# Performance work log

Hardware: AMD Instinct MI355X
Metric: run time of the kernel (lower is better)

The kernel has to match this reference:

```python
import jax, jax.numpy as jnp
import numpy as np

BATCH, SEQ, H_IN, N_STATE, H_OUT = 16, 4096, 128, 256, 128
RMIN, RMAX, MAX_PHASE = 0.9, 1.0, 6.283


def setup_inputs() -> dict:
    key = jax.random.key(0)
    ks = jax.random.split(key, 9)
    u = jax.random.normal(ks[0], (BATCH, SEQ, H_IN), jnp.float32)
    # LRU exponential parameterization init (matches torch __init__)
    u1 = jax.random.uniform(ks[1], (N_STATE,), jnp.float32)
    u2 = jax.random.uniform(ks[2], (N_STATE,), jnp.float32)
    nu_log = jnp.log(-0.5 * jnp.log(u1 * (RMAX + RMIN) * (RMAX - RMIN) + RMIN ** 2))
    theta_log = jnp.log(MAX_PHASE * u2)
    lam_abs = jnp.exp(-jnp.exp(nu_log))
    gamma_log = jnp.log(jnp.sqrt(1.0 - lam_abs ** 2))
    s2in = np.sqrt(2.0 * H_IN).astype(np.float32)
    B_re = jax.random.normal(ks[3], (N_STATE, H_IN), jnp.float32) / s2in
    B_im = jax.random.normal(ks[4], (N_STATE, H_IN), jnp.float32) / s2in
    sst = np.sqrt(float(N_STATE)).astype(np.float32)
    C_re = jax.random.normal(ks[5], (H_OUT, N_STATE), jnp.float32) / sst
    C_im = jax.random.normal(ks[6], (H_OUT, N_STATE), jnp.float32) / sst
    D = jax.random.normal(ks[7], (H_OUT, H_IN), jnp.float32) / np.sqrt(float(H_IN)).astype(np.float32)
    return dict(u=u, nu_log=nu_log, theta_log=theta_log, gamma_log=gamma_log,
                B_re=B_re, B_im=B_im, C_re=C_re, C_im=C_im, D=D)


def _combine(a, b):
    # complex affine composition: (l, x) o (l', x') -> (l*l', l'*x + x')
    l1r, l1i, x1r, x1i = a
    l2r, l2i, x2r, x2i = b
    lr = l1r * l2r - l1i * l2i
    li = l1r * l2i + l1i * l2r
    xr = l2r * x1r - l2i * x1i + x2r
    xi = l2r * x1i + l2i * x1r + x2i
    return (lr, li, xr, xi)


def reference(u, nu_log, theta_log, gamma_log, B_re, B_im, C_re, C_im, D):
    lam_mod = jnp.exp(-jnp.exp(nu_log))          # |lambda|, [N]
    th = jnp.exp(theta_log)
    lam_re = lam_mod * jnp.cos(th)
    lam_im = lam_mod * jnp.sin(th)
    gammas = jnp.exp(gamma_log)                  # [N]
    # input projection Bu_t = gamma * (B @ u_t), complex -> real/imag parts
    Bu_re = jnp.einsum('blh,nh->bln', u, B_re) * gammas  # [B,L,N]
    Bu_im = jnp.einsum('blh,nh->bln', u, B_im) * gammas
    Bsz, L, N = Bu_re.shape
    lr = jnp.broadcast_to(lam_re, (Bsz, L, N))
    li = jnp.broadcast_to(lam_im, (Bsz, L, N))
    # parallel scan of x_t = lambda * x_{t-1} + Bu_t, x0 = 0
    _, _, xr, xi = jax.lax.associative_scan(_combine, (lr, li, Bu_re, Bu_im), axis=1)
    zero = jnp.zeros((Bsz, 1, N), u.dtype)
    pre_re = jnp.concatenate([zero, xr[:, :-1]], axis=1)  # states[:, :-1]
    pre_im = jnp.concatenate([zero, xi[:, :-1]], axis=1)
    # y_t = Re(C x_{t-1}) + D u_t
    y = (jnp.einsum('bln,on->blo', pre_re, C_re)
         - jnp.einsum('bln,on->blo', pre_im, C_im)
         + jnp.einsum('blh,oh->blo', u, D))
    return y
```

## Files before the change

### kernel.cpp

```cpp
#include <hip/hip_runtime.h>
#include <math.h>

#define BATCH 16
#define SEQ   4096
#define HIN   128
#define NST   256
#define HOUT  128
#define CL    32
#define NC    (SEQ/CL)
#define ROWS  (BATCH*SEQ)
#define KTOT  640
#define NPRE  512

typedef __attribute__((ext_vector_type(8))) short short8;
typedef __attribute__((ext_vector_type(4))) float f32x4;

__device__ inline unsigned short f2bf(float f) {
  union { float f; unsigned u; } v; v.f = f;
  unsigned r = v.u + 0x7FFFu + ((v.u >> 16) & 1u);
  return (unsigned short)(r >> 16);
}
__device__ inline float bf2f(unsigned short s) {
  union { unsigned u; float f; } v; v.u = ((unsigned)s) << 16;
  return v.f;
}

__global__ __launch_bounds__(256) void k_prep(
    const float* __restrict__ nu_log, const float* __restrict__ theta_log,
    const float* __restrict__ gamma_log,
    const float* __restrict__ Bre, const float* __restrict__ Bim,
    const float* __restrict__ Cre, const float* __restrict__ Cim,
    const float* __restrict__ Dm,
    float* __restrict__ lamre, float* __restrict__ lamim,
    float* __restrict__ lamPowRe, float* __restrict__ lamPowIm,
    unsigned short* __restrict__ Wb, unsigned short* __restrict__ W) {
  int idx = blockIdx.x*256 + threadIdx.x;
  if (idx < NST) {
    float lm = expf(-expf(nu_log[idx]));
    float th = expf(theta_log[idx]);
    float lr = lm * cosf(th), li = lm * sinf(th);
    lamre[idx] = lr; lamim[idx] = li;
    float pr = 1.f, pi = 0.f;
    for (int j = 0; j < CL; ++j) {
      lamPowRe[j*NST + idx] = pr;
      lamPowIm[j*NST + idx] = pi;
      float nr = pr*lr - pi*li;
      float ni = pr*li + pi*lr;
      pr = nr; pi = ni;
    }
  }
  if (idx < 512*HIN) {
    int r = idx >> 7, h = idx & 127;
    int g = r >> 7;
    int w = r & 127;
    int n = g*64 + (w & 63);
    float gm = expf(gamma_log[n]);
    float v = (w < 64) ? Bre[n*HIN + h] : Bim[n*HIN + h];
    Wb[idx] = f2bf(gm * v);
  }
  if (idx < HOUT*KTOT) {
    int o = idx / KTOT, k = idx - o*KTOT;
    float v;
    if (k < NST)        v =  Cre[o*NST + k];
    else if (k < 2*NST) v = -Cim[o*NST + (k - NST)];
    else                v =  Dm[o*HIN + (k - 2*NST)];
    W[idx] = f2bf(v);
  }
}

__global__ __launch_bounds__(256) void k_cast(
    const float* __restrict__ u, unsigned short* __restrict__ ubf) {
  size_t i = (size_t)(blockIdx.x*256 + threadIdx.x) * 4;
  float4 v = *(const float4*)(u + i);
  ushort4 o;
  o.x = f2bf(v.x); o.y = f2bf(v.y); o.z = f2bf(v.z); o.w = f2bf(v.w);
  *(ushort4*)(ubf + i) = o;
}

union SharedBu {
  unsigned short B[128][136];
  float stg[2][32][132];
};
__global__ __launch_bounds__(256) void k_bu(
    const unsigned short* __restrict__ ubf, const unsigned short* __restrict__ Wb,
    const float* __restrict__ lamre, const float* __restrict__ lamim,
    unsigned short* __restrict__ preL,
    float* __restrict__ S_re, float* __restrict__ S_im) {
  __shared__ unsigned short Asl[128][136];
  __shared__ SharedBu sh;
  int tid = threadIdx.x;
  int row0 = blockIdx.x * 128;
  int wid = tid >> 6, lane = tid & 63;
  int lm = lane & 15, lq = lane >> 4;
  int m0 = (wid >> 1) * 64, n0 = (wid & 1) * 64;
  int b = row0 >> 12;
  int cbase = (row0 & 4095) >> 5;
#pragma unroll
  for (int cc = 0; cc < 8; ++cc) {
    int ch = cc*256 + tid;
    int r = ch >> 4, h0 = (ch & 15) * 8;
    *(short8*)&Asl[r][h0] = *(const short8*)&ubf[(size_t)(row0 + r)*HIN + h0];
  }
  for (int g = 0; g < 4; ++g) {
    __syncthreads();
#pragma unroll
    for (int cc = 0; cc < 8; ++cc) {
      int ch = cc*256 + tid;
      int r = ch >> 4, h0 = (ch & 15) * 8;
      *(short8*)&sh.B[r][h0] = *(const short8*)&Wb[(size_t)(g*128 + r)*HIN + h0];
    }
    __syncthreads();
    f32x4 acc[4][4];
#pragma unroll
    for (int i = 0; i < 4; ++i)
#pragma unroll
      for (int j = 0; j < 4; ++j) acc[i][j] = (f32x4)0.f;
#pragma unroll
    for (int ks = 0; ks < 4; ++ks) {
      int k0 = ks*32 + lq*8;
      short8 a[4], bb[4];
#pragma unroll
      for (int i = 0; i < 4; ++i) a[i] = *(const short8*)&Asl[m0 + i*16 + lm][k0];
#pragma unroll
      for (int j = 0; j < 4; ++j) bb[j] = *(const short8*)&sh.B[n0 + j*16 + lm][k0];
#pragma unroll
      for (int i = 0; i < 4; ++i)
#pragma unroll
        for (int j = 0; j < 4; ++j)
          acc[i][j] = __builtin_amdgcn_mfma_f32_16x16x32_bf16(a[i], bb[j], acc[i][j], 0, 0, 0);
    }
    for (int p = 0; p < 2; ++p) {
      __syncthreads();
#pragma unroll
      for (int ii = 0; ii < 2; ++ii) {
        int i = 2*p + ii;
#pragma unroll
        for (int j = 0; j < 4; ++j)
#pragma unroll
          for (int r = 0; r < 4; ++r) {
            int trow = ii*16 + lq*4 + r;
            sh.stg[wid >> 1][trow][n0 + j*16 + lm] = acc[i][j][r];
          }
      }
      __syncthreads();
      if (tid < 128) {
        int buf = tid >> 6, nl = tid & 63;
        int ng = g*64 + nl;
        float lr = lamre[ng], li = lamim[ng];
        float rr[CL], ri[CL];
#pragma unroll
        for (int t = 0; t < CL; ++t) {
          rr[t] = sh.stg[buf][t][nl];
          ri[t] = sh.stg[buf][t][64 + nl];
        }
        int rowb = row0 + buf*64 + p*32;
        unsigned short* pl = preL + (size_t)rowb*NPRE;
        float sr = 0.f, si = 0.f;
#pragma unroll
        for (int t = 0; t < CL; ++t) {
          pl[ng]       = f2bf(sr);
          pl[NST + ng] = f2bf(si);
          float nr = lr*sr - li*si + rr[t];
          float ni = lr*si + li*sr + ri[t];
          sr = nr; si = ni; pl += NPRE;
        }
        int c = cbase + buf*2 + p;
        int idx = (b*NC + c)*NST + ng;
        S_re[idx] = sr; S_im[idx] = si;
      }
    }
  }
}

__global__ __launch_bounds__(256) void k_carry2(
    const float* __restrict__ S_re, const float* __restrict__ S_im,
    const float* __restrict__ lamre, const float* __restrict__ lamim,
    float* __restrict__ G_re, float* __restrict__ G_im) {
  int blk = blockIdx.x;
  int b = blk >> 3, g = blk & 7;
  int n = threadIdx.x;
  float ar = lamre[n], ai = lamim[n];
#pragma unroll
  for (int s = 0; s < 5; ++s) { float nr = ar*ar - ai*ai, ni = 2.f*ar*ai; ar = nr; ai = ni; }
  float tr = 0.f, ti = 0.f;
#pragma unroll
  for (int cc = 0; cc < 16; ++cc) {
    int idx = (b*NC + g*16 + cc)*NST + n;
    float nr = ar*tr - ai*ti + S_re[idx];
    float ni = ar*ti + ai*tr + S_im[idx];
    tr = nr; ti = ni;
  }
  int gi = (b*8 + g)*NST + n;
  G_re[gi] = tr; G_im[gi] = ti;
}

__global__ __launch_bounds__(256) void k_final(
    const float* __restrict__ S_re, const float* __restrict__ S_im,
    const float* __restrict__ G_re, const float* __restrict__ G_im,
    const float* __restrict__ lamre, const float* __restrict__ lamim,
    float* __restrict__ X0_re, float* __restrict__ X0_im) {
  int blk = blockIdx.x;
  int b = blk >> 3, g = blk & 7;
  int n = threadIdx.x;
  float ar = lamre[n], ai = lamim[n];
#pragma unroll
  for (int s = 0; s < 5; ++s) { float nr = ar*ar - ai*ai, ni = 2.f*ar*ai; ar = nr; ai = ni; }
  float a5r = ar, a5i = ai;
#pragma unroll
  for (int s = 0; s < 4; ++s) { float nr = a5r*a5r - a5i*a5i, ni = 2.f*a5r*a5i; a5r = nr; a5i = ni; }
  float pr = 0.f, pi = 0.f;
  for (int j = 0; j < g; ++j) {
    int gi = (b*8 + j)*NST + n;
    float nr = a5r*pr - a5i*pi + G_re[gi];
    float ni = a5r*pi + a5i*pr + G_im[gi];
    pr = nr; pi = ni;
  }
  float xr = pr, xi = pi;
#pragma unroll
  for (int cc = 0; cc < 16; ++cc) {
    int idx = (b*NC + g*16 + cc)*NST + n;
    X0_re[idx] = xr; X0_im[idx] = xi;
    float nr = ar*xr - ai*xi + S_re[idx];
    float ni = ar*xi + ai*xr + S_im[idx];
    xr = nr; xi = ni;
  }
}

__global__ __launch_bounds__(256) void k_out2(
    const unsigned short* __restrict__ preL, const unsigned short* __restrict__ ubf,
    const unsigned short* __restrict__ W,
    const float* __restrict__ lamPowRe, const float* __restrict__ lamPowIm,
    const float* __restrict__ X0_re, const float* __restrict__ X0_im,
    float* __restrict__ y) {
  __shared__ unsigned short Asl[128][136];
  __shared__ unsigned short Bsl[128][136];
  int tid = threadIdx.x;
  int row0 = blockIdx.x * 128;
  int wid = tid >> 6, lane = tid & 63;
  int lm = lane & 15, lq = lane >> 4;
  int m0 = (wid >> 1) * 64, n0 = (wid & 1) * 64;
  f32x4 acc[4][4];
#pragma unroll
  for (int i = 0; i < 4; ++i)
#pragma unroll
    for (int j = 0; j < 4; ++j) acc[i][j] = (f32x4)0.f;
  for (int s = 0; s < 5; ++s) {
#pragma unroll
    for (int cc = 0; cc < 8; ++cc) {
      int ch = cc*256 + tid;
      int r = ch >> 4, h0 = (ch & 15) * 8;
      if (s < 4) {
        int row = row0 + r;
        int j = row & 31, cidx = row >> 5;
        int n = ((s & 1) << 7) + h0;
        short8 loc = *(const short8*)&preL[(size_t)row*NPRE + s*128 + h0];
        float lre[8], lim_[8], x0r[8], x0i[8];
        *(float4*)&lre[0]  = *(const float4*)&lamPowRe[j*NST + n];
        *(float4*)&lre[4]  = *(const float4*)&lamPowRe[j*NST + n + 4];
        *(float4*)&lim_[0] = *(const float4*)&lamPowIm[j*NST + n];
        *(float4*)&lim_[4] = *(const float4*)&lamPowIm[j*NST + n + 4];
        *(float4*)&x0r[0]  = *(const float4*)&X0_re[cidx*NST + n];
        *(float4*)&x0r[4]  = *(const float4*)&X0_re[cidx*NST + n + 4];
        *(float4*)&x0i[0]  = *(const float4*)&X0_im[cidx*NST + n];
        *(float4*)&x0i[4]  = *(const float4*)&X0_im[cidx*NST + n + 4];
        unsigned short o[8];
#pragma unroll
        for (int e = 0; e < 8; ++e) {
          float lv = bf2f((unsigned short)loc[e]);
          float v = (s < 2) ? (lv + lre[e]*x0r[e] - lim_[e]*x0i[e])
                            : (lv + lre[e]*x0i[e] + lim_[e]*x0r[e]);
          o[e] = f2bf(v);
        }
        *(short8*)&Asl[r][h0] = *(const short8*)o;
      } else {
        *(short8*)&Asl[r][h0] = *(const short8*)&ubf[(size_t)(row0 + r)*HIN + h0];
      }
      *(short8*)&Bsl[r][h0] = *(const short8*)&W[(size_t)r*KTOT + s*128 + h0];
    }
    __syncthreads();
#pragma unroll
    for (int ks = 0; ks < 4; ++ks) {
      int k0 = ks*32 + lq*8;
      short8 a[4], bb[4];
#pragma unroll
      for (int i = 0; i < 4; ++i) a[i] = *(const short8*)&Asl[m0 + i*16 + lm][k0];
#pragma unroll
      for (int j = 0; j < 4; ++j) bb[j] = *(const short8*)&Bsl[n0 + j*16 + lm][k0];
#pragma unroll
      for (int i = 0; i < 4; ++i)
#pragma unroll
        for (int j = 0; j < 4; ++j)
          acc[i][j] = __builtin_amdgcn_mfma_f32_16x16x32_bf16(a[i], bb[j], acc[i][j], 0, 0, 0);
    }
    __syncthreads();
  }
#pragma unroll
  for (int i = 0; i < 4; ++i)
#pragma unroll
    for (int j = 0; j < 4; ++j)
#pragma unroll
      for (int r = 0; r < 4; ++r)
        y[(size_t)(row0 + m0 + i*16 + lq*4 + r)*HOUT + n0 + j*16 + lm] = acc[i][j][r];
}

extern "C" void kernel_launch(void* const* d_in, const int* in_sizes, int n_in,
                              void* d_out, int out_size, void* d_ws, size_t ws_size,
                              hipStream_t stream) {
  const float* u         = (const float*)d_in[0];
  const float* nu_log    = (const float*)d_in[1];
  const float* theta_log = (const float*)d_in[2];
  const float* gamma_log = (const float*)d_in[3];
  const float* B_re      = (const float*)d_in[4];
  const float* B_im      = (const float*)d_in[5];
  const float* C_re      = (const float*)d_in[6];
  const float* C_im      = (const float*)d_in[7];
  const float* Dm        = (const float*)d_in[8];
  float* y = (float*)d_out;
  char* ws = (char*)d_ws;

  float*          lamre    = (float*)(ws);
  float*          lamim    = (float*)(ws + 1024);
  float*          lamPowRe = (float*)(ws + 4096);
  float*          lamPowIm = (float*)(ws + 4096 + 32768);
  unsigned short* ubf      = (unsigned short*)(ws + 69632);
  unsigned short* Wb       = (unsigned short*)(ws + 69632 + 16777216);
  unsigned short* W        = (unsigned short*)(ws + 69632 + 16777216 + 131072);
  unsigned short* preL     = (unsigned short*)(ws + 69632 + 16777216 + 131072 + 163840);
  char* p2 = ws + 69632 + 16777216 + 131072 + 163840 + (size_t)ROWS*NPRE*2;
  float* S_re  = (float*)(p2);
  float* S_im  = (float*)(p2 + 2097152);
  float* G_re  = (float*)(p2 + 2*2097152);
  float* G_im  = (float*)(p2 + 2*2097152 + 131072);
  float* X0_re = (float*)(p2 + 2*2097152 + 2*131072);
  float* X0_im = (float*)(p2 + 3*2097152 + 2*131072);

  k_prep<<<320, 256, 0, stream>>>(nu_log, theta_log, gamma_log, B_re, B_im,
                                  C_re, C_im, Dm, lamre, lamim,
                                  lamPowRe, lamPowIm, Wb, W);
  k_cast<<<(ROWS*HIN)/1024, 256, 0, stream>>>(u, ubf);
  k_bu<<<ROWS/128, 256, 0, stream>>>(ubf, Wb, lamre, lamim, preL, S_re, S_im);
  k_carry2<<<BATCH*8, 256, 0, stream>>>(S_re, S_im, lamre, lamim, G_re, G_im);
  k_final<<<BATCH*8, 256, 0, stream>>>(S_re, S_im, G_re, G_im, lamre, lamim,
                                       X0_re, X0_im);
  k_out2<<<ROWS/128, 256, 0, stream>>>(preL, ubf, W, lamPowRe, lamPowIm,
                                       X0_re, X0_im, y);
}
```

Measured before the change: 181.0 us.

## Fuse bf16 cast into GEMMs, pack lambda/X0 as bf16 pairs, register-load A tiles

Drops the separate u-to-bf16 cast kernel: k_bu and k_out2 now read fp32 u directly and convert it in-kernel. Lambda powers and chunk carry states are stored as packed bf16 re/im pairs, halving their footprint and load count. k_out2 builds its A fragments straight from global memory into registers instead of staging them in LDS. Each wave now covers 32 rows by all 128 output columns. This lowers LDS use and global traffic but reads u twice in fp32 and issues uncoalesced per-lane global loads inside the MFMA loop. It also loses precision on lambda powers and carry states.

```diff
diff --git a/kernel.cpp b/kernel.cpp
--- a/kernel.cpp
+++ b/kernel.cpp
@@ -24,6 +24,9 @@
   union { unsigned u; float f; } v; v.u = ((unsigned)s) << 16;
   return v.f;
 }
+__device__ inline float bits2f(unsigned u) {
+  union { unsigned u; float f; } v; v.u = u; return v.f;
+}
 
 __global__ __launch_bounds__(256) void k_prep(
     const float* __restrict__ nu_log, const float* __restrict__ theta_log,
@@ -32,7 +35,7 @@
     const float* __restrict__ Cre, const float* __restrict__ Cim,
     const float* __restrict__ Dm,
     float* __restrict__ lamre, float* __restrict__ lamim,
-    float* __restrict__ lamPowRe, float* __restrict__ lamPowIm,
+    unsigned* __restrict__ lamPk,
     unsigned short* __restrict__ Wb, unsigned short* __restrict__ W) {
   int idx = blockIdx.x*256 + threadIdx.x;
   if (idx < NST) {
@@ -42,8 +45,7 @@
     lamre[idx] = lr; lamim[idx] = li;
     float pr = 1.f, pi = 0.f;
     for (int j = 0; j < CL; ++j) {
-      lamPowRe[j*NST + idx] = pr;
-      lamPowIm[j*NST + idx] = pi;
+      lamPk[j*NST + idx] = ((unsigned)f2bf(pi) << 16) | (unsigned)f2bf(pr);
       float nr = pr*lr - pi*li;
       float ni = pr*li + pi*lr;
       pr = nr; pi = ni;
@@ -68,21 +70,12 @@
   }
 }
 
-__global__ __launch_bounds__(256) void k_cast(
-    const float* __restrict__ u, unsigned short* __restrict__ ubf) {
-  size_t i = (size_t)(blockIdx.x*256 + threadIdx.x) * 4;
-  float4 v = *(const float4*)(u + i);
-  ushort4 o;
-  o.x = f2bf(v.x); o.y = f2bf(v.y); o.z = f2bf(v.z); o.w = f2bf(v.w);
-  *(ushort4*)(ubf + i) = o;
-}
-
 union SharedBu {
   unsigned short B[128][136];
   float stg[2][32][132];
 };
 __global__ __launch_bounds__(256) void k_bu(
-    const unsigned short* __restrict__ ubf, const unsigned short* __restrict__ Wb,
+    const float* __restrict__ u, const unsigned short* __restrict__ Wb,
     const float* __restrict__ lamre, const float* __restrict__ lamim,
     unsigned short* __restrict__ preL,
     float* __restrict__ S_re, float* __restrict__ S_im) {
@@ -99,7 +92,13 @@
   for (int cc = 0; cc < 8; ++cc) {
     int ch = cc*256 + tid;
     int r = ch >> 4, h0 = (ch & 15) * 8;
-    *(short8*)&Asl[r][h0] = *(const short8*)&ubf[(size_t)(row0 + r)*HIN + h0];
+    const float* src = u + (size_t)(row0 + r)*HIN + h0;
+    float4 v0 = *(const float4*)src;
+    float4 v1 = *(const float4*)(src + 4);
+    unsigned short o[8];
+    o[0]=f2bf(v0.x); o[1]=f2bf(v0.y); o[2]=f2bf(v0.z); o[3]=f2bf(v0.w);
+    o[4]=f2bf(v1.x); o[5]=f2bf(v1.y); o[6]=f2bf(v1.z); o[7]=f2bf(v1.w);
+    *(short8*)&Asl[r][h0] = *(const short8*)o;
   }
   for (int g = 0; g < 4; ++g) {
     __syncthreads();
@@ -198,7 +197,7 @@
     const float* __restrict__ S_re, const float* __restrict__ S_im,
     const float* __restrict__ G_re, const float* __restrict__ G_im,
     const float* __restrict__ lamre, const float* __restrict__ lamim,
-    float* __restrict__ X0_re, float* __restrict__ X0_im) {
+    unsigned* __restrict__ X0Pk) {
   int blk = blockIdx.x;
   int b = blk >> 3, g = blk & 7;
   int n = threadIdx.x;
@@ -219,7 +218,7 @@
 #pragma unroll
   for (int cc = 0; cc < 16; ++cc) {
     int idx = (b*NC + g*16 + cc)*NST + n;
-    X0_re[idx] = xr; X0_im[idx] = xi;
+    X0Pk[idx] = ((unsigned)f2bf(xi) << 16) | (unsigned)f2bf(xr);
     float nr = ar*xr - ai*xi + S_re[idx];
     float ni = ar*xi + ai*xr + S_im[idx];
     xr = nr; xi = ni;
@@ -227,80 +226,93 @@
 }
 
 __global__ __launch_bounds__(256) void k_out2(
-    const unsigned short* __restrict__ preL, const unsigned short* __restrict__ ubf,
+    const unsigned short* __restrict__ preL, const float* __restrict__ u,
     const unsigned short* __restrict__ W,
-    const float* __restrict__ lamPowRe, const float* __restrict__ lamPowIm,
-    const float* __restrict__ X0_re, const float* __restrict__ X0_im,
+    const unsigned* __restrict__ lamPk, const unsigned* __restrict__ X0Pk,
     float* __restrict__ y) {
-  __shared__ unsigned short Asl[128][136];
   __shared__ unsigned short Bsl[128][136];
   int tid = threadIdx.x;
   int row0 = blockIdx.x * 128;
   int wid = tid >> 6, lane = tid & 63;
   int lm = lane & 15, lq = lane >> 4;
-  int m0 = (wid >> 1) * 64, n0 = (wid & 1) * 64;
-  f32x4 acc[4][4];
-#pragma unroll
-  for (int i = 0; i < 4; ++i)
-#pragma unroll
-    for (int j = 0; j < 4; ++j) acc[i][j] = (f32x4)0.f;
+  int m0 = wid * 32;
+  f32x4 acc[2][8];
+#pragma unroll
+  for (int i = 0; i < 2; ++i)
+#pragma unroll
+    for (int j = 0; j < 8; ++j) acc[i][j] = (f32x4)0.f;
+  int grow[2];
+  grow[0] = row0 + m0 + lm;
+  grow[1] = grow[0] + 16;
   for (int s = 0; s < 5; ++s) {
 #pragma unroll
     for (int cc = 0; cc < 8; ++cc) {
       int ch = cc*256 + tid;
       int r = ch >> 4, h0 = (ch & 15) * 8;
-      if (s < 4) {
-        int row = row0 + r;
-        int j = row & 31, cidx = row >> 5;
-        int n = ((s & 1) << 7) + h0;
-        short8 loc = *(const short8*)&preL[(size_t)row*NPRE + s*128 + h0];
-        float lre[8], lim_[8], x0r[8], x0i[8];
-        *(float4*)&lre[0]  = *(const float4*)&lamPowRe[j*NST + n];
-        *(float4*)&lre[4]  = *(const float4*)&lamPowRe[j*NST + n + 4];
-        *(float4*)&lim_[0] = *(const float4*)&lamPowIm[j*NST + n];
-        *(float4*)&lim_[4] = *(const float4*)&lamPowIm[j*NST + n + 4];
-        *(float4*)&x0r[0]  = *(const float4*)&X0_re[cidx*NST + n];
-        *(float4*)&x0r[4]  = *(const float4*)&X0_re[cidx*NST + n + 4];
-        *(float4*)&x0i[0]  = *(const float4*)&X0_im[cidx*NST + n];
-        *(float4*)&x0i[4]  = *(const float4*)&X0_im[cidx*NST + n + 4];
-        unsigned short o[8];
-#pragma unroll
-        for (int e = 0; e < 8; ++e) {
-          float lv = bf2f((unsigned short)loc[e]);
-          float v = (s < 2) ? (lv + lre[e]*x0r[e] - lim_[e]*x0i[e])
-                            : (lv + lre[e]*x0i[e] + lim_[e]*x0r[e]);
-          o[e] = f2bf(v);
-        }
-        *(short8*)&Asl[r][h0] = *(const short8*)o;
-      } else {
-        *(short8*)&Asl[r][h0] = *(const short8*)&ubf[(size_t)(row0 + r)*HIN + h0];
-      }
       *(short8*)&Bsl[r][h0] = *(const short8*)&W[(size_t)r*KTOT + s*128 + h0];
     }
     __syncthreads();
 #pragma unroll
     for (int ks = 0; ks < 4; ++ks) {
       int k0 = ks*32 + lq*8;
-      short8 a[4], bb[4];
-#pragma unroll
-      for (int i = 0; i < 4; ++i) a[i] = *(const short8*)&Asl[m0 + i*16 + lm][k0];
-#pragma unroll
-      for (int j = 0; j < 4; ++j) bb[j] = *(const short8*)&Bsl[n0 + j*16 + lm][k0];
-#pragma unroll
-      for (int i = 0; i < 4; ++i)
-#pragma unroll
-        for (int j = 0; j < 4; ++j)
+      short8 a[2];
+      if (s < 4) {
+        int n = ((s & 1) << 7) + k0;
+#pragma unroll
+        for (int i = 0; i < 2; ++i) {
+          int gr = grow[i];
+          int j32 = gr & 31, cidx = gr >> 5;
+          short8 loc = *(const short8*)&preL[(size_t)gr*NPRE + s*128 + k0];
+          uint4 lp0 = *(const uint4*)&lamPk[j32*NST + n];
+          uint4 lp1 = *(const uint4*)&lamPk[j32*NST + n + 4];
+          uint4 xp0 = *(const uint4*)&X0Pk[cidx*NST + n];
+          uint4 xp1 = *(const uint4*)&X0Pk[cidx*NST + n + 4];
+          unsigned lps[8] = {lp0.x, lp0.y, lp0.z, lp0.w, lp1.x, lp1.y, lp1.z, lp1.w};
+          unsigned xps[8] = {xp0.x, xp0.y, xp0.z, xp0.w, xp1.x, xp1.y, xp1.z, xp1.w};
+          unsigned short o[8];
+#pragma unroll
+          for (int e = 0; e < 8; ++e) {
+            float lr = bits2f(lps[e] << 16);
+            float li = bits2f(lps[e] & 0xFFFF0000u);
+            float xr = bits2f(xps[e] << 16);
+            float xi = bits2f(xps[e] & 0xFFFF0000u);
+            float lv = bf2f((unsigned short)loc[e]);
+            float v = (s < 2) ? (lv + lr*xr - li*xi)
+                              : (lv + lr*xi + li*xr);
+            o[e] = f2bf(v);
+          }
+          a[i] = *(const short8*)o;
+        }
+      } else {
+#pragma unroll
+        for (int i = 0; i < 2; ++i) {
+          const float* src = u + (size_t)grow[i]*HIN + k0;
+          float4 v0 = *(const float4*)src;
+          float4 v1 = *(const float4*)(src + 4);
+          unsigned short o[8];
+          o[0]=f2bf(v0.x); o[1]=f2bf(v0.y); o[2]=f2bf(v0.z); o[3]=f2bf(v0.w);
+          o[4]=f2bf(v1.x); o[5]=f2bf(v1.y); o[6]=f2bf(v1.z); o[7]=f2bf(v1.w);
+          a[i] = *(const short8*)o;
+        }
+      }
+      short8 bb[8];
+#pragma unroll
+      for (int j = 0; j < 8; ++j) bb[j] = *(const short8*)&Bsl[j*16 + lm][k0];
+#pragma unroll
+      for (int i = 0; i < 2; ++i)
+#pragma unroll
+        for (int j = 0; j < 8; ++j)
           acc[i][j] = __builtin_amdgcn_mfma_f32_16x16x32_bf16(a[i], bb[j], acc[i][j], 0, 0, 0);
     }
     __syncthreads();
   }
 #pragma unroll
-  for (int i = 0; i < 4; ++i)
-#pragma unroll
-    for (int j = 0; j < 4; ++j)
+  for (int i = 0; i < 2; ++i)
+#pragma unroll
+    for (int j = 0; j < 8; ++j)
 #pragma unroll
       for (int r = 0; r < 4; ++r)
-        y[(size_t)(row0 + m0 + i*16 + lq*4 + r)*HOUT + n0 + j*16 + lm] = acc[i][j][r];
+        y[(size_t)(row0 + m0 + i*16 + lq*4 + r)*HOUT + j*16 + lm] = acc[i][j][r];
 }
 
 extern "C" void kernel_launch(void* const* d_in, const int* in_sizes, int n_in,
@@ -318,30 +330,23 @@
   float* y = (float*)d_out;
   char* ws = (char*)d_ws;
 
-  float*          lamre    = (float*)(ws);
-  float*          lamim    = (float*)(ws + 1024);
-  float*          lamPowRe = (float*)(ws + 4096);
-  float*          lamPowIm = (float*)(ws + 4096 + 32768);
-  unsigned short* ubf      = (unsigned short*)(ws + 69632);
-  unsigned short* Wb       = (unsigned short*)(ws + 69632 + 16777216);
-  unsigned short* W        = (unsigned short*)(ws + 69632 + 16777216 + 131072);
-  unsigned short* preL     = (unsigned short*)(ws + 69632 + 16777216 + 131072 + 163840);
-  char* p2 = ws + 69632 + 16777216 + 131072 + 163840 + (size_t)ROWS*NPRE*2;
-  float* S_re  = (float*)(p2);
-  float* S_im  = (float*)(p2 + 2097152);
-  float* G_re  = (float*)(p2 + 2*2097152);
-  float* G_im  = (float*)(p2 + 2*2097152 + 131072);
-  float* X0_re = (float*)(p2 + 2*2097152 + 2*131072);
-  float* X0_im = (float*)(p2 + 3*2097152 + 2*131072);
+  size_t off = 0;
+  float* lamre = (float*)(ws + off);            off += 1024;
+  float* lamim = (float*)(ws + off);            off += 1024;
+  unsigned* lamPk = (unsigned*)(ws + off);      off += 32768;
+  unsigned short* Wb = (unsigned short*)(ws + off); off += 131072;
+  unsigned short* W  = (unsigned short*)(ws + off); off += 163840;
+  unsigned short* preL = (unsigned short*)(ws + off); off += (size_t)ROWS*NPRE*2;
+  float* S_re = (float*)(ws + off);             off += 2097152;
+  float* S_im = (float*)(ws + off);             off += 2097152;
+  float* G_re = (float*)(ws + off);             off += 131072;
+  float* G_im = (float*)(ws + off);             off += 131072;
+  unsigned* X0Pk = (unsigned*)(ws + off);       off += 2097152;
 
   k_prep<<<320, 256, 0, stream>>>(nu_log, theta_log, gamma_log, B_re, B_im,
-                                  C_re, C_im, Dm, lamre, lamim,
-                                  lamPowRe, lamPowIm, Wb, W);
-  k_cast<<<(ROWS*HIN)/1024, 256, 0, stream>>>(u, ubf);
-  k_bu<<<ROWS/128, 256, 0, stream>>>(ubf, Wb, lamre, lamim, preL, S_re, S_im);
+                                  C_re, C_im, Dm, lamre, lamim, lamPk, Wb, W);
+  k_bu<<<ROWS/128, 256, 0, stream>>>(u, Wb, lamre, lamim, preL, S_re, S_im);
   k_carry2<<<BATCH*8, 256, 0, stream>>>(S_re, S_im, lamre, lamim, G_re, G_im);
-  k_final<<<BATCH*8, 256, 0, stream>>>(S_re, S_im, G_re, G_im, lamre, lamim,
-                                       X0_re, X0_im);
-  k_out2<<<ROWS/128, 256, 0, stream>>>(preL, ubf, W, lamPowRe, lamPowIm,
-                                       X0_re, X0_im, y);
-}
+  k_final<<<BATCH*8, 256, 0, stream>>>(S_re, S_im, G_re, G_im, lamre, lamim, X0Pk);
+  k_out2<<<ROWS/128, 256, 0, stream>>>(preL, u, W, lamPk, X0Pk, y);
+}
```

Measured after the change: 172.3 us. 4.8% less time.
